# Kernel tuning notes

Measured on AMD Instinct MI355X. Metric: run time of the kernel, lower is better.

## Reference

```python
import jax, jax.numpy as jnp
import numpy as np

EMBED = 1024
HEADS = 16
HEAD_DIM = EMBED // HEADS
OUT = 1024


def setup_inputs() -> dict:
    key = jax.random.key(0)
    ks = jax.random.split(key, 6)
    x = jax.random.normal(ks[0], (4, 2048, EMBED), dtype=jnp.float32)
    # per-head projection weights, torch Linear convention: [out_features, in_features]
    s = 1.0 / np.sqrt(HEAD_DIM)
    Wv = jax.random.uniform(ks[1], (HEAD_DIM, HEAD_DIM), jnp.float32, -s, s)
    Wk = jax.random.uniform(ks[2], (HEAD_DIM, HEAD_DIM), jnp.float32, -s, s)
    Wq = jax.random.uniform(ks[3], (HEAD_DIM, HEAD_DIM), jnp.float32, -s, s)
    so = 1.0 / np.sqrt(EMBED)
    Wo = jax.random.uniform(ks[4], (OUT, EMBED), jnp.float32, -so, so)
    bo = jax.random.uniform(ks[5], (OUT,), jnp.float32, -so, so)
    return {"x": x, "Wq": Wq, "Wk": Wk, "Wv": Wv, "Wo": Wo, "bo": bo}


def reference(x, Wq, Wk, Wv, Wo, bo):
    N, L, _ = x.shape
    xh = x.reshape(N, L, HEADS, HEAD_DIM)  # nqhd
    q = jnp.einsum('nqhd,ed->nqhe', xh, Wq)
    k = jnp.einsum('nkhd,ed->nkhe', xh, Wk)
    v = jnp.einsum('nkhd,ed->nkhe', xh, Wv)
    # full score matrix [N, H, Q, K], scaled by sqrt(embed_size) as in source
    energy = jnp.einsum('nqhd,nkhd->nhqk', q, k) / np.sqrt(EMBED).astype(np.float32)
    attn = jax.nn.softmax(energy, axis=3)
    out = jnp.einsum('nhqk,nkhd->nqhd', attn, v).reshape(N, L, EMBED)
    return out @ Wo.T + bo
```

## Files before the change

kernel.cpp:

```cpp
#include <hip/hip_runtime.h>
#include <hip/hip_bf16.h>
#include <stdint.h>
#include <stddef.h>


typedef __attribute__((ext_vector_type(8))) short bf16x8;
typedef __attribute__((ext_vector_type(4))) float f32x4;
typedef __attribute__((ext_vector_type(4))) short short4v;
typedef __attribute__((ext_vector_type(2))) uint32_t uint2v;

__device__ __forceinline__ f32x4 mfma16(bf16x8 a, bf16x8 b, f32x4 c) {
    return __builtin_amdgcn_mfma_f32_16x16x32_bf16(a, b, c, 0, 0, 0);
}

__device__ __forceinline__ short f2bf(float x) {
    union { float f; uint32_t u; } v; v.f = x;
    uint32_t r = (v.u + 0x7FFFu + ((v.u >> 16) & 1u)) >> 16;
    return (short)(uint16_t)r;
}

__device__ __forceinline__ uint32_t pk2bf(float a, float b) {
    union { __hip_bfloat162 h; uint32_t u; } v;
    v.h = __float22bfloat162_rn(float2{a, b});
    return v.u;
}

__device__ __forceinline__ bf16x8 cvt8(const float* __restrict__ p) {
    f32x4 a = *(const f32x4*)p;
    f32x4 b = *(const f32x4*)(p + 4);
    bf16x8 r;
    r[0] = f2bf(a[0]); r[1] = f2bf(a[1]); r[2] = f2bf(a[2]); r[3] = f2bf(a[3]);
    r[4] = f2bf(b[0]); r[5] = f2bf(b[1]); r[6] = f2bf(b[2]); r[7] = f2bf(b[3]);
    return r;
}

__global__ __launch_bounds__(256)
void kvproj_kernel(const float* __restrict__ x, const float* __restrict__ Wk,
                   const float* __restrict__ Wv, short* __restrict__ kf_ws,
                   short* __restrict__ vf_ws) {
    __shared__ alignas(16) short kbuf[128 * 72];
    __shared__ alignas(16) short vbuf[64 * 136];
    int tid = threadIdx.x;
    int lt = blockIdx.x & 15, nh = blockIdx.x >> 4;
    int n = nh >> 4, h = nh & 15;
    int l0 = lt * 128, kt0 = lt * 2;
    int wv = tid >> 6, lane = tid & 63, quad = lane >> 4, lc = lane & 15;

    for (int u = tid; u < 1024; u += 256) {
        int r = u >> 3, c = (u & 7) * 8;
        *(bf16x8*)(kbuf + r * 72 + c) =
            cvt8(x + (size_t)(n * 2048 + l0 + r) * 1024 + h * 64 + c);
    }
    __syncthreads();

    bf16x8 xa[2][2];
    for (int mt = 0; mt < 2; ++mt)
        for (int kf = 0; kf < 2; ++kf)
            xa[mt][kf] = *(bf16x8*)(kbuf + (wv * 32 + mt * 16 + lc) * 72 + kf * 32 + quad * 8);

    f32x4 ka[2][4] = {}, va[2][4] = {};
    for (int nt = 0; nt < 4; ++nt)
        for (int kf = 0; kf < 2; ++kf) {
            bf16x8 wkb = cvt8(Wk + (nt * 16 + lc) * 64 + kf * 32 + quad * 8);
            bf16x8 wvb = cvt8(Wv + (nt * 16 + lc) * 64 + kf * 32 + quad * 8);
            for (int mt = 0; mt < 2; ++mt) {
                ka[mt][nt] = mfma16(xa[mt][kf], wkb, ka[mt][nt]);
                va[mt][nt] = mfma16(xa[mt][kf], wvb, va[mt][nt]);
            }
        }

    for (int mt = 0; mt < 2; ++mt) {
        int off = wv * 32 + mt * 16;
        for (int nt = 0; nt < 4; ++nt)
            for (int i = 0; i < 4; ++i) {
                float kv = ka[mt][nt][i], vv = va[mt][nt][i];
                kbuf[(off + quad * 4 + i) * 72 + nt * 16 + lc] = f2bf(kv);
                vbuf[(nt * 16 + lc) * 136 + off + quad * 4 + i] = f2bf(vv);
            }
    }
    __syncthreads();

    size_t base = (size_t)nh * 131072 + (size_t)kt0 * 4096;
    for (int u = tid; u < 1024; u += 256) {
        int tile = u >> 9, rem = u & 511, seg = rem >> 6, ln = u & 63;
        int t = seg >> 1, kf = seg & 1;
        int lq = ln >> 4, ll = ln & 15;
        bf16x8 kw = *(bf16x8*)(kbuf + (tile * 64 + t * 16 + ll) * 72 + kf * 32 + lq * 8);
        *(bf16x8*)(kf_ws + base + (size_t)tile * 4096 + seg * 512 + ln * 8) = kw;
        bf16x8 vw = *(bf16x8*)(vbuf + (t * 16 + ll) * 136 + tile * 64 + kf * 32 + lq * 8);
        *(bf16x8*)(vf_ws + base + (size_t)tile * 4096 + seg * 512 + ln * 8) = vw;
    }
}

__global__ __launch_bounds__(256, 2)
void flash_kernel(const float* __restrict__ x, const float* __restrict__ Wq,
                  const short* __restrict__ kf_ws, const short* __restrict__ vf_ws,
                  short* __restrict__ ao) {
    __shared__ alignas(16) short pbuf[256 * 72];
    int tid = threadIdx.x;
    int nh = blockIdx.x & 63, qt = blockIdx.x >> 6;
    int n = nh >> 4, h = nh & 15;
    int q0 = qt * 256;
    int wv = tid >> 6, lane = tid & 63, quad = lane >> 4, lc = lane & 15;

    for (int u = tid; u < 2048; u += 256) {
        int r = u >> 3, c = (u & 7) * 8;
        *(bf16x8*)(pbuf + r * 72 + c) =
            cvt8(x + (size_t)(n * 2048 + q0 + r) * 1024 + h * 64 + c);
    }
    __syncthreads();
    {
        bf16x8 xa[4][2];
        for (int mt = 0; mt < 4; ++mt)
            for (int kf = 0; kf < 2; ++kf)
                xa[mt][kf] = *(bf16x8*)(pbuf + (wv * 64 + mt * 16 + lc) * 72 +
                                        kf * 32 + quad * 8);
        f32x4 qacc[4][4] = {};
        for (int nt = 0; nt < 4; ++nt)
            for (int kf = 0; kf < 2; ++kf) {
                bf16x8 wb = cvt8(Wq + (nt * 16 + lc) * 64 + kf * 32 + quad * 8);
                for (int mt = 0; mt < 4; ++mt)
                    qacc[mt][nt] = mfma16(xa[mt][kf], wb, qacc[mt][nt]);
            }
        const float QS = 0.04508422002778011f;
        for (int mt = 0; mt < 4; ++mt)
            for (int nt = 0; nt < 4; ++nt)
                for (int i = 0; i < 4; ++i)
                    pbuf[(wv * 64 + mt * 16 + quad * 4 + i) * 72 + nt * 16 + lc] =
                        f2bf(qacc[mt][nt][i] * QS);
    }
    bf16x8 qa[4][2];
    for (int mt = 0; mt < 4; ++mt)
        for (int kf = 0; kf < 2; ++kf)
            qa[mt][kf] = *(bf16x8*)(pbuf + (wv * 64 + mt * 16 + lc) * 72 +
                                    kf * 32 + quad * 8);

    f32x4 o[4][4] = {};
    float lsum[4] = {0.f, 0.f, 0.f, 0.f};
    const short* kbase = kf_ws + (size_t)nh * 131072 + lane * 8;
    const short* vbase = vf_ws + (size_t)nh * 131072 + lane * 8;

    for (int kt = 0; kt < 32; ++kt) {
        const short* kp = kbase + (size_t)kt * 4096;
        const short* vp = vbase + (size_t)kt * 4096;
        bf16x8 kA[4][2];
#pragma unroll
        for (int t = 0; t < 4; ++t)
            for (int kf = 0; kf < 2; ++kf)
                kA[t][kf] = *(const bf16x8*)(kp + (t * 2 + kf) * 512);
        f32x4 s[4][4] = {};
#pragma unroll
        for (int t = 0; t < 4; ++t)
            for (int q2 = 0; q2 < 4; ++q2) {
                s[q2][t] = mfma16(kA[t][0], qa[q2][0], s[q2][t]);
                s[q2][t] = mfma16(kA[t][1], qa[q2][1], s[q2][t]);
            }
        bf16x8 vA[4][2];
#pragma unroll
        for (int dt = 0; dt < 4; ++dt)
            for (int kf = 0; kf < 2; ++kf)
                vA[dt][kf] = *(const bf16x8*)(vp + (dt * 2 + kf) * 512);
#pragma unroll
        for (int q2 = 0; q2 < 4; ++q2) {
            int prow = (wv * 64 + q2 * 16 + lc) * 72;
            float ts = 0.f;
#pragma unroll
            for (int t = 0; t < 4; ++t) {
                float p0 = __builtin_amdgcn_exp2f(s[q2][t][0]);
                float p1 = __builtin_amdgcn_exp2f(s[q2][t][1]);
                float p2 = __builtin_amdgcn_exp2f(s[q2][t][2]);
                float p3 = __builtin_amdgcn_exp2f(s[q2][t][3]);
                ts += (p0 + p1) + (p2 + p3);
                uint2v w = {pk2bf(p0, p1), pk2bf(p2, p3)};
                *(uint2v*)(pbuf + prow + t * 16 + quad * 4) = w;
            }
            lsum[q2] += ts;
        }
#pragma unroll
        for (int q2 = 0; q2 < 4; ++q2)
            for (int kf = 0; kf < 2; ++kf) {
                bf16x8 pB = *(bf16x8*)(pbuf + (wv * 64 + q2 * 16 + lc) * 72 +
                                       kf * 32 + quad * 8);
                for (int dt = 0; dt < 4; ++dt)
                    o[q2][dt] = mfma16(vA[dt][kf], pB, o[q2][dt]);
            }
    }

    for (int q2 = 0; q2 < 4; ++q2) {
        float t = lsum[q2];
        t += __shfl_xor(t, 16, 64);
        t += __shfl_xor(t, 32, 64);
        float inv = 1.f / t;
        int q = q0 + wv * 64 + q2 * 16 + lc;
        for (int dt = 0; dt < 4; ++dt) {
            short4v pk;
            for (int i = 0; i < 4; ++i) pk[i] = f2bf(o[q2][dt][i] * inv);
            *(short4v*)(ao + (size_t)(n * 2048 + q) * 1024 + h * 64 +
                        dt * 16 + quad * 4) = pk;
        }
    }
}

__global__ __launch_bounds__(256)
void outgemm_kernel(const short* __restrict__ A, const float* __restrict__ Wo,
                    const float* __restrict__ bo, float* __restrict__ out) {
    __shared__ alignas(16) short at[128 * 40];
    __shared__ alignas(16) short bt[128 * 40];
    int tid = threadIdx.x;
    int bm = blockIdx.x >> 3, bn = blockIdx.x & 7;
    int m0 = bm * 128, n0 = bn * 128;
    int wv = tid >> 6, lane = tid & 63, quad = lane >> 4, lc = lane & 15;
    int wr = wv >> 1, wc = wv & 1;

    int r1 = tid >> 2, c1 = (tid & 3) * 8;
    int u2 = tid + 256;
    int r2 = u2 >> 2, c2 = (u2 & 3) * 8;

    f32x4 acc[4][4] = {};
    for (int kt = 0; kt < 32; ++kt) {
        int k0 = kt * 32;
        bf16x8 a0 = *(const bf16x8*)(A + (size_t)(m0 + r1) * 1024 + k0 + c1);
        bf16x8 a1 = *(const bf16x8*)(A + (size_t)(m0 + r2) * 1024 + k0 + c2);
        bf16x8 b0 = cvt8(Wo + (size_t)(n0 + r1) * 1024 + k0 + c1);
        bf16x8 b1 = cvt8(Wo + (size_t)(n0 + r2) * 1024 + k0 + c2);
        __syncthreads();
        *(bf16x8*)(at + r1 * 40 + c1) = a0;
        *(bf16x8*)(at + r2 * 40 + c2) = a1;
        *(bf16x8*)(bt + r1 * 40 + c1) = b0;
        *(bf16x8*)(bt + r2 * 40 + c2) = b1;
        __syncthreads();
        bf16x8 af[4], bfr[4];
        for (int mt = 0; mt < 4; ++mt)
            af[mt] = *(bf16x8*)(at + (wr * 64 + mt * 16 + lc) * 40 + quad * 8);
        for (int nt = 0; nt < 4; ++nt)
            bfr[nt] = *(bf16x8*)(bt + (wc * 64 + nt * 16 + lc) * 40 + quad * 8);
        for (int mt = 0; mt < 4; ++mt)
            for (int nt = 0; nt < 4; ++nt)
                acc[mt][nt] = mfma16(af[mt], bfr[nt], acc[mt][nt]);
    }
    for (int nt = 0; nt < 4; ++nt) {
        float bv = bo[n0 + wc * 64 + nt * 16 + lc];
        for (int mt = 0; mt < 4; ++mt)
            for (int i = 0; i < 4; ++i) {
                int m = m0 + wr * 64 + mt * 16 + quad * 4 + i;
                int nn = n0 + wc * 64 + nt * 16 + lc;
                out[(size_t)m * 1024 + nn] = acc[mt][nt][i] + bv;
            }
    }
}

extern "C" void kernel_launch(void* const* d_in, const int* in_sizes, int n_in,
                              void* d_out, int out_size, void* d_ws, size_t ws_size,
                              hipStream_t stream) {
    const float* x  = (const float*)d_in[0];
    const float* Wq = (const float*)d_in[1];
    const float* Wk = (const float*)d_in[2];
    const float* Wv = (const float*)d_in[3];
    const float* Wo = (const float*)d_in[4];
    const float* bo = (const float*)d_in[5];
    float* out = (float*)d_out;

    short* kf_ws = (short*)d_ws;
    short* vf_ws = kf_ws + 8388608;
    short* ao_ws = vf_ws + 8388608;

    kvproj_kernel<<<dim3(1024), dim3(256), 0, stream>>>(x, Wk, Wv, kf_ws, vf_ws);
    flash_kernel<<<dim3(512), dim3(256), 0, stream>>>(x, Wq, kf_ws, vf_ws, ao_ws);
    outgemm_kernel<<<dim3(512), dim3(256), 0, stream>>>(ao_ws, Wo, bo, out);
}
```

Measured before the change: 234.4 us.

## Store attention output and Wo in MFMA fragment layout, drop LDS staging in out-GEMM

```diff
diff --git a/kernel.cpp b/kernel.cpp
--- a/kernel.cpp
+++ b/kernel.cpp
@@ -71,12 +71,14 @@
 
     for (int mt = 0; mt < 2; ++mt) {
         int off = wv * 32 + mt * 16;
-        for (int nt = 0; nt < 4; ++nt)
+        for (int nt = 0; nt < 4; ++nt) {
+            short4v pv;
             for (int i = 0; i < 4; ++i) {
-                float kv = ka[mt][nt][i], vv = va[mt][nt][i];
-                kbuf[(off + quad * 4 + i) * 72 + nt * 16 + lc] = f2bf(kv);
-                vbuf[(nt * 16 + lc) * 136 + off + quad * 4 + i] = f2bf(vv);
-            }
+                kbuf[(off + quad * 4 + i) * 72 + nt * 16 + lc] = f2bf(ka[mt][nt][i]);
+                pv[i] = f2bf(va[mt][nt][i]);
+            }
+            *(short4v*)(vbuf + (nt * 16 + lc) * 136 + off + quad * 4) = pv;
+        }
     }
     __syncthreads();
 
@@ -191,49 +193,53 @@
         t += __shfl_xor(t, 16, 64);
         t += __shfl_xor(t, 32, 64);
         float inv = 1.f / t;
-        int q = q0 + wv * 64 + q2 * 16 + lc;
+        int mtile = (n * 2048 + q0) / 16 + wv * 4 + q2;
         for (int dt = 0; dt < 4; ++dt) {
+            int kseg = h * 2 + (dt >> 1);
+            int qd8 = ((dt & 1) * 4 + quad) >> 1;
             short4v pk;
             for (int i = 0; i < 4; ++i) pk[i] = f2bf(o[q2][dt][i] * inv);
-            *(short4v*)(ao + (size_t)(n * 2048 + q) * 1024 + h * 64 +
-                        dt * 16 + quad * 4) = pk;
+            *(short4v*)(ao + (size_t)(mtile * 32 + kseg) * 512 +
+                        (qd8 * 16 + lc) * 8 + (quad & 1) * 4) = pk;
         }
     }
 }
 
 __global__ __launch_bounds__(256)
-void outgemm_kernel(const short* __restrict__ A, const float* __restrict__ Wo,
+void wopack_kernel(const float* __restrict__ Wo, short* __restrict__ wfb) {
+    int idx = blockIdx.x * 256 + threadIdx.x;
+    int nrow = idx >> 7;
+    int k0 = (idx & 127) * 8;
+    bf16x8 v = cvt8(Wo + (size_t)nrow * 1024 + k0);
+    int ntile = nrow >> 4, lcn = nrow & 15;
+    int kseg = k0 >> 5, qd = (k0 >> 3) & 3;
+    *(bf16x8*)(wfb + ((size_t)(ntile * 32 + kseg) * 64 + qd * 16 + lcn) * 8) = v;
+}
+
+__global__ __launch_bounds__(256)
+void outgemm_kernel(const short* __restrict__ afb, const short* __restrict__ wfb,
                     const float* __restrict__ bo, float* __restrict__ out) {
-    __shared__ alignas(16) short at[128 * 40];
-    __shared__ alignas(16) short bt[128 * 40];
     int tid = threadIdx.x;
-    int bm = blockIdx.x >> 3, bn = blockIdx.x & 7;
+    int bm = blockIdx.x & 63, bn = blockIdx.x >> 6;
     int m0 = bm * 128, n0 = bn * 128;
     int wv = tid >> 6, lane = tid & 63, quad = lane >> 4, lc = lane & 15;
     int wr = wv >> 1, wc = wv & 1;
-
-    int r1 = tid >> 2, c1 = (tid & 3) * 8;
-    int u2 = tid + 256;
-    int r2 = u2 >> 2, c2 = (u2 & 3) * 8;
+    int mtb = bm * 8 + wr * 4;
+    int ntb = bn * 8 + wc * 4;
+
+    const short* ab = afb + lane * 8;
+    const short* bb = wfb + lane * 8;
 
     f32x4 acc[4][4] = {};
     for (int kt = 0; kt < 32; ++kt) {
-        int k0 = kt * 32;
-        bf16x8 a0 = *(const bf16x8*)(A + (size_t)(m0 + r1) * 1024 + k0 + c1);
-        bf16x8 a1 = *(const bf16x8*)(A + (size_t)(m0 + r2) * 1024 + k0 + c2);
-        bf16x8 b0 = cvt8(Wo + (size_t)(n0 + r1) * 1024 + k0 + c1);
-        bf16x8 b1 = cvt8(Wo + (size_t)(n0 + r2) * 1024 + k0 + c2);
-        __syncthreads();
-        *(bf16x8*)(at + r1 * 40 + c1) = a0;
-        *(bf16x8*)(at + r2 * 40 + c2) = a1;
-        *(bf16x8*)(bt + r1 * 40 + c1) = b0;
-        *(bf16x8*)(bt + r2 * 40 + c2) = b1;
-        __syncthreads();
         bf16x8 af[4], bfr[4];
-        for (int mt = 0; mt < 4; ++mt)
-            af[mt] = *(bf16x8*)(at + (wr * 64 + mt * 16 + lc) * 40 + quad * 8);
+#pragma unroll
+        for (int mt = 0; mt < 4; ++mt)
+            af[mt] = *(const bf16x8*)(ab + ((size_t)(mtb + mt) * 32 + kt) * 512);
+#pragma unroll
         for (int nt = 0; nt < 4; ++nt)
-            bfr[nt] = *(bf16x8*)(bt + (wc * 64 + nt * 16 + lc) * 40 + quad * 8);
+            bfr[nt] = *(const bf16x8*)(bb + ((size_t)(ntb + nt) * 32 + kt) * 512);
+#pragma unroll
         for (int mt = 0; mt < 4; ++mt)
             for (int nt = 0; nt < 4; ++nt)
                 acc[mt][nt] = mfma16(af[mt], bfr[nt], acc[mt][nt]);
@@ -263,8 +269,10 @@
     short* kf_ws = (short*)d_ws;
     short* vf_ws = kf_ws + 8388608;
     short* ao_ws = vf_ws + 8388608;
+    short* wf_ws = kf_ws;
 
     kvproj_kernel<<<dim3(1024), dim3(256), 0, stream>>>(x, Wk, Wv, kf_ws, vf_ws);
     flash_kernel<<<dim3(512), dim3(256), 0, stream>>>(x, Wq, kf_ws, vf_ws, ao_ws);
-    outgemm_kernel<<<dim3(512), dim3(256), 0, stream>>>(ao_ws, Wo, bo, out);
-}
+    wopack_kernel<<<dim3(512), dim3(256), 0, stream>>>(Wo, wf_ws);
+    outgemm_kernel<<<dim3(512), dim3(256), 0, stream>>>(ao_ws, wf_ws, bo, out);
+}
```

Measured after the change: 223.8 us. -4.6%, faster.
